# Optimization experiments

Measured on AMD Instinct MI355X. Metric: run time of the kernel, lower is better.

## Reference

```python
import jax, jax.numpy as jnp
import numpy as np
import math

H = 1024        # number of SSM copies (d_model)
N_HALF = 32     # stored state size (N//2 due to conjugate symmetry)
CHANNELS = 1
SEQ_L = 4096
DT_MIN, DT_MAX = 1e-3, 1e-1


def setup_inputs() -> dict:
    key = jax.random.key(0)
    k1, k2, k3, k4, k5 = jax.random.split(key, 5)
    # log_dt ~ Uniform[log(dt_min), log(dt_max)] as in SSKernel.__init__
    log_dt = jax.random.uniform(k1, (H,), dtype=jnp.float32) \
        * (math.log(DT_MAX) - math.log(DT_MIN)) + math.log(DT_MIN)
    # complex params stored as real (..., 2) views (torch.view_as_real)
    B_ri = jax.random.normal(k2, (H, N_HALF, 2), dtype=jnp.float32)
    C_ri = jax.random.normal(k3, (CHANNELS, H, N_HALF, 2), dtype=jnp.float32)
    # inv_A_real = log(-clamp(A_real, max=-1e-4)); sample A_real ~ -0.5 (S4D-Lin)
    inv_A_real = jnp.log(0.5 * jnp.ones((H, N_HALF), dtype=jnp.float32))
    inv_A_real = inv_A_real + 0.01 * jax.random.normal(k4, (H, N_HALF), dtype=jnp.float32)
    # A_imag = pi * n (S4D-Lin init)
    A_imag = jnp.tile(math.pi * jnp.arange(N_HALF, dtype=jnp.float32), (H, 1))
    A_imag = A_imag + 0.01 * jax.random.normal(k5, (H, N_HALF), dtype=jnp.float32)
    return {"log_dt": log_dt, "B_ri": B_ri, "C_ri": C_ri,
            "inv_A_real": inv_A_real, "A_imag": A_imag, "L": SEQ_L}


def _r2c(x):
    return jax.lax.complex(x[..., 0], x[..., 1])


def reference(log_dt, B_ri, C_ri, inv_A_real, A_imag, L):
    """SSKernelDiag.forward (S4D, bilinear discretization, state=None, rate=1)."""
    dt = jnp.exp(log_dt)                       # (H,)
    C = _r2c(C_ri)                             # (C, H, N) complex
    B = _r2c(B_ri)                             # (H, N) complex
    A = -jnp.exp(inv_A_real) + 1j * A_imag     # (H, N) complex
    dtA = A * dt[:, None]                      # (H, N)
    # C <- (B * C) / (1 - dtA/2) * dt
    C_eff = (B[None] * C) * (1.0 / (1.0 - dtA / 2)) * dt[:, None]  # (C, H, N)
    dA = (1.0 + dtA / 2) / (1.0 - dtA / 2)     # (H, N) bilinear transform
    log_dA = jnp.log(dA)
    # log-Vandermonde: K[c,h,l] = 2 * Re( sum_n C_eff[c,h,n] * dA[h,n]^l )
    ell = jnp.arange(L, dtype=jnp.float32)
    V = jnp.exp(log_dA[:, :, None] * ell)      # (H, N, L) complex
    K = 2.0 * jnp.einsum('chn,hnl->chl', C_eff, V).real  # (C, H, L) float32
    return K
```

## Files before the change

### kernel.cpp

```cpp
#include <hip/hip_runtime.h>


#define HDIM    1024
#define NSTATE  32
#define SEQ_L   4096
#define TPB     256
#define JCOUNT  (SEQ_L / TPB)

__global__ __launch_bounds__(TPB) void sskernel_diag(
    const float* __restrict__ log_dt,
    const float* __restrict__ B_ri,
    const float* __restrict__ C_ri,
    const float* __restrict__ inv_A_real,
    const float* __restrict__ A_imag,
    float* __restrict__ out)
{
    __shared__ float4 s_loR[NSTATE][16];
    __shared__ float4 s_hh[NSTATE][16];

    const int h   = blockIdx.x;
    const int tid = threadIdx.x;

    if (tid < 2 * NSTATE) {
        const int n    = tid & (NSTATE - 1);
        const int role = tid >> 5;
        const int idx  = h * NSTATE + n;

        const float dt   = expf(log_dt[h]);
        const float Ar   = -expf(inv_A_real[idx]);
        const float Ai   = A_imag[idx];
        const float dtAr = Ar * dt;
        const float dtAi = Ai * dt;

        const float dr = 1.0f - 0.5f * dtAr;
        const float di =       -0.5f * dtAi;
        const float inv_den = 1.0f / (dr * dr + di * di);

        const float nr = 1.0f + 0.5f * dtAr;
        const float ni =        0.5f * dtAi;
        const float dAr = (nr * dr + ni * di) * inv_den;
        const float dAi = (ni * dr - nr * di) * inv_den;

        if (role == 0) {
            float sr = dAr, si = dAi;
            #pragma unroll
            for (int t = 0; t < 8; ++t) {
                const float tr = sr * sr - si * si;
                si = 2.0f * sr * si;
                sr = tr;
            }
            const float recx = 2.0f * sr;
            const float recy = -(sr * sr + si * si);

            const float br = B_ri[2 * idx], bi = B_ri[2 * idx + 1];
            const float cr = C_ri[2 * idx], ci = C_ri[2 * idx + 1];
            const float bcr = br * cr - bi * ci;
            const float bci = br * ci + bi * cr;
            const float scale = 2.0f * dt * inv_den;
            float pr = (bcr * dr + bci * di) * scale;
            float pi = (bci * dr - bcr * di) * scale;

            #pragma unroll
            for (int t = 0; t < 16; ++t) {
                s_loR[n][t] = make_float4(pr, pi, recx, recy);
                const float tr = pr * dAr - pi * dAi;
                pi = pr * dAi + pi * dAr;
                pr = tr;
            }
        } else {
            float er = dAr, ei = dAi;
            #pragma unroll
            for (int t = 0; t < 4; ++t) {
                const float tr = er * er - ei * ei;
                ei = 2.0f * er * ei;
                er = tr;
            }
            float sr = er, si = ei;
            #pragma unroll
            for (int t = 0; t < 4; ++t) {
                const float tr = sr * sr - si * si;
                si = 2.0f * sr * si;
                sr = tr;
            }
            float qr = 1.0f, qi = 0.0f;
            #pragma unroll
            for (int u = 0; u < 16; ++u) {
                s_hh[n][u] = make_float4(qr, qi,
                                         qr * sr - qi * si,
                                         qr * si + qi * sr);
                const float tr = qr * er - qi * ei;
                qi = qr * ei + qi * er;
                qr = tr;
            }
        }
    }
    __syncthreads();

    float acc[JCOUNT];
    #pragma unroll
    for (int j = 0; j < JCOUNT; ++j) acc[j] = 0.0f;

    const int i_lo = tid & 15;
    const int i_hi = tid >> 4;

    #pragma unroll 4
    for (int n = 0; n < NSTATE; ++n) {
        const float4 LR = s_loR[n][i_lo];
        const float4 HH = s_hh[n][i_hi];

        float c0 = LR.x * HH.x - LR.y * HH.y;
        float c1 = LR.x * HH.z - LR.y * HH.w;
        acc[0] += c0;
        acc[1] += c1;

        #pragma unroll
        for (int j = 2; j < JCOUNT; ++j) {
            const float c2 = LR.z * c1 + LR.w * c0;
            acc[j] += c2;
            c0 = c1;
            c1 = c2;
        }
    }

    float* o = out + (size_t)h * SEQ_L + tid;
    #pragma unroll
    for (int j = 0; j < JCOUNT; ++j) o[j * TPB] = acc[j];
}

extern "C" void kernel_launch(void* const* d_in, const int* in_sizes, int n_in,
                              void* d_out, int out_size, void* d_ws, size_t ws_size,
                              hipStream_t stream) {
    const float* log_dt     = (const float*)d_in[0];
    const float* B_ri       = (const float*)d_in[1];
    const float* C_ri       = (const float*)d_in[2];
    const float* inv_A_real = (const float*)d_in[3];
    const float* A_imag     = (const float*)d_in[4];
    float* out = (float*)d_out;

    sskernel_diag<<<HDIM, TPB, 0, stream>>>(log_dt, B_ri, C_ri,
                                            inv_A_real, A_imag, out);
}
```

Baseline: 84.72 us.

## Pair state modes into float2 lanes and halve threads per block

Halves the block to 128 threads so each thread computes 32 outputs. State modes are interleaved in pairs so the second-order recurrence runs two independent chains side by side in float2 accumulators, which could map to packed FP32 math and gives more ILP. The shared tables are rebuilt for the new stride (128 instead of 256) and the pair layout. The tradeoff is twice the accumulator registers per thread and half as many threads per block.

Result: no change. 85.40 us (+0.8%).

```diff
diff --git a/kernel.cpp b/kernel.cpp
--- a/kernel.cpp
+++ b/kernel.cpp
@@ -3,8 +3,9 @@
 
 #define HDIM    1024
 #define NSTATE  32
+#define NPAIR   (NSTATE / 2)
 #define SEQ_L   4096
-#define TPB     256
+#define TPB     128
 #define JCOUNT  (SEQ_L / TPB)
 
 __global__ __launch_bounds__(TPB) void sskernel_diag(
@@ -15,8 +16,10 @@
     const float* __restrict__ A_imag,
     float* __restrict__ out)
 {
-    __shared__ float4 s_loR[NSTATE][16];
-    __shared__ float4 s_hh[NSTATE][16];
+    __shared__ float4 s_loA[NPAIR][16];
+    __shared__ float4 s_g[NPAIR][8];
+    __shared__ float4 s_gs[NPAIR][8];
+    __shared__ float4 s_rec[NPAIR];
 
     const int h   = blockIdx.x;
     const int tid = threadIdx.x;
@@ -24,6 +27,8 @@
     if (tid < 2 * NSTATE) {
         const int n    = tid & (NSTATE - 1);
         const int role = tid >> 5;
+        const int p    = n >> 1;
+        const int q    = n & 1;
         const int idx  = h * NSTATE + n;
 
         const float dt   = expf(log_dt[h]);
@@ -44,13 +49,14 @@
         if (role == 0) {
             float sr = dAr, si = dAi;
             #pragma unroll
-            for (int t = 0; t < 8; ++t) {
+            for (int t = 0; t < 7; ++t) {
                 const float tr = sr * sr - si * si;
                 si = 2.0f * sr * si;
                 sr = tr;
             }
-            const float recx = 2.0f * sr;
-            const float recy = -(sr * sr + si * si);
+            float* rec = (float*)&s_rec[p];
+            rec[q]     = 2.0f * sr;
+            rec[2 + q] = -(sr * sr + si * si);
 
             const float br = B_ri[2 * idx], bi = B_ri[2 * idx + 1];
             const float cr = C_ri[2 * idx], ci = C_ri[2 * idx + 1];
@@ -62,7 +68,9 @@
 
             #pragma unroll
             for (int t = 0; t < 16; ++t) {
-                s_loR[n][t] = make_float4(pr, pi, recx, recy);
+                float* e = (float*)&s_loA[p][t];
+                e[q]     = pr;
+                e[2 + q] = pi;
                 const float tr = pr * dAr - pi * dAi;
                 pi = pr * dAi + pi * dAr;
                 pr = tr;
@@ -77,17 +85,20 @@
             }
             float sr = er, si = ei;
             #pragma unroll
-            for (int t = 0; t < 4; ++t) {
+            for (int t = 0; t < 3; ++t) {
                 const float tr = sr * sr - si * si;
                 si = 2.0f * sr * si;
                 sr = tr;
             }
             float qr = 1.0f, qi = 0.0f;
             #pragma unroll
-            for (int u = 0; u < 16; ++u) {
-                s_hh[n][u] = make_float4(qr, qi,
-                                         qr * sr - qi * si,
-                                         qr * si + qi * sr);
+            for (int u = 0; u < 8; ++u) {
+                float* eg  = (float*)&s_g[p][u];
+                float* egs = (float*)&s_gs[p][u];
+                eg[q]      = qr;
+                eg[2 + q]  = qi;
+                egs[q]     = qr * sr - qi * si;
+                egs[2 + q] = qr * si + qi * sr;
                 const float tr = qr * er - qi * ei;
                 qi = qr * ei + qi * er;
                 qr = tr;
@@ -96,35 +107,40 @@
     }
     __syncthreads();
 
-    float acc[JCOUNT];
+    float2 acc[JCOUNT];
     #pragma unroll
-    for (int j = 0; j < JCOUNT; ++j) acc[j] = 0.0f;
+    for (int j = 0; j < JCOUNT; ++j) acc[j] = make_float2(0.0f, 0.0f);
 
     const int i_lo = tid & 15;
     const int i_hi = tid >> 4;
 
-    #pragma unroll 4
-    for (int n = 0; n < NSTATE; ++n) {
-        const float4 LR = s_loR[n][i_lo];
-        const float4 HH = s_hh[n][i_hi];
+    #pragma unroll 2
+    for (int p = 0; p < NPAIR; ++p) {
+        const float4 LA = s_loA[p][i_lo];
+        const float4 G  = s_g[p][i_hi];
+        const float4 GS = s_gs[p][i_hi];
+        const float4 RC = s_rec[p];
 
-        float c0 = LR.x * HH.x - LR.y * HH.y;
-        float c1 = LR.x * HH.z - LR.y * HH.w;
-        acc[0] += c0;
-        acc[1] += c1;
+        float c0x = LA.x * G.x  - LA.z * G.z;
+        float c0y = LA.y * G.y  - LA.w * G.w;
+        float c1x = LA.x * GS.x - LA.z * GS.z;
+        float c1y = LA.y * GS.y - LA.w * GS.w;
+        acc[0].x += c0x;  acc[0].y += c0y;
+        acc[1].x += c1x;  acc[1].y += c1y;
 
         #pragma unroll
         for (int j = 2; j < JCOUNT; ++j) {
-            const float c2 = LR.z * c1 + LR.w * c0;
-            acc[j] += c2;
-            c0 = c1;
-            c1 = c2;
+            const float c2x = RC.x * c1x + RC.z * c0x;
+            const float c2y = RC.y * c1y + RC.w * c0y;
+            acc[j].x += c2x;  acc[j].y += c2y;
+            c0x = c1x;  c0y = c1y;
+            c1x = c2x;  c1y = c2y;
         }
     }
 
     float* o = out + (size_t)h * SEQ_L + tid;
     #pragma unroll
-    for (int j = 0; j < JCOUNT; ++j) o[j * TPB] = acc[j];
+    for (int j = 0; j < JCOUNT; ++j) o[j * TPB] = acc[j].x + acc[j].y;
 }
 
 extern "C" void kernel_launch(void* const* d_in, const int* in_sizes, int n_in,
```
